# Performance work log

Measured on AMD Instinct MI355X. Metric: run time of the kernel, lower is better.

## Reference

```python
import jax, jax.numpy as jnp
import numpy as np

B = 4096
N_PATCH = 196  # 14x14 patches of a 28x28 image
THRESHOLD = 0.9
SECONDARY = 0.5
SECONDARY_WEIGHT = 0.5

_CNOT = jnp.array([[1, 0, 0, 0], [0, 1, 0, 0], [0, 0, 0, 1], [0, 0, 1, 0]], dtype=jnp.complex64)


def _ry(t):
    c, s = jnp.cos(t / 2), jnp.sin(t / 2)
    m = jnp.stack([jnp.stack([c, -s], -1), jnp.stack([s, c], -1)], -2)
    return m.astype(jnp.complex64)


def _rx(t):
    c, s = jnp.cos(t / 2), jnp.sin(t / 2)
    z = jnp.zeros_like(c)
    re = jnp.stack([jnp.stack([c, z], -1), jnp.stack([z, c], -1)], -2)
    im = jnp.stack([jnp.stack([z, -s], -1), jnp.stack([-s, z], -1)], -2)
    return (re + 1j * im).astype(jnp.complex64)


def _rz(t):
    em = jnp.exp(-0.5j * t.astype(jnp.complex64) if hasattr(t, 'astype') else -0.5j * t)
    ep = jnp.conj(em)
    z = jnp.zeros_like(em)
    m = jnp.stack([jnp.stack([em, z], -1), jnp.stack([z, ep], -1)], -2)
    return m.astype(jnp.complex64)


def _apply_1q(state, mat, wire):
    # state: (P, 2, 2, 2, 2); mat: (2,2) shared or (P,2,2) per-sample
    s = jnp.moveaxis(state, 1 + wire, -1)
    if mat.ndim == 2:
        s = jnp.einsum('pabcj,ij->pabci', s, mat)
    else:
        s = jnp.einsum('pabcj,pij->pabci', s, mat)
    return jnp.moveaxis(s, -1, 1 + wire)


def _apply_2q(state, mat4, w0, w1):
    s = jnp.moveaxis(state, (1 + w0, 1 + w1), (-2, -1))
    shp = s.shape
    s = s.reshape(shp[:-2] + (4,))
    s = jnp.einsum('...j,ij->...i', s, mat4)
    return jnp.moveaxis(s.reshape(shp), (-2, -1), (1 + w0, 1 + w1))


def _quantum_measure(angles, q_params):
    # angles: (P, 4) real -> Pauli-Z expectations (P, 4)
    P = angles.shape[0]
    state = jnp.zeros((P, 2, 2, 2, 2), jnp.complex64).at[:, 0, 0, 0, 0].set(1.0)
    # GeneralEncoder: RY(pixel) on each wire
    for w in range(4):
        state = _apply_1q(state, _ry(angles[:, w]), w)
    # fixed 'RandomLayer' (8 ops, deterministic gate sequence, trainable params)
    state = _apply_1q(state, _rx(q_params[0]), 0)
    state = _apply_1q(state, _ry(q_params[1]), 1)
    state = _apply_1q(state, _rz(q_params[2]), 2)
    state = _apply_2q(state, _CNOT, 0, 1)
    state = _apply_1q(state, _rx(q_params[3]), 3)
    state = _apply_2q(state, _CNOT, 2, 3)
    state = _apply_1q(state, _ry(q_params[4]), 0)
    state = _apply_1q(state, _rz(q_params[5]), 3)
    probs = state.real ** 2 + state.imag ** 2
    exps = []
    for w in range(4):
        p = jnp.moveaxis(probs, 1 + w, 1)
        exps.append((p[:, 0] - p[:, 1]).reshape(P, -1).sum(-1))
    return jnp.stack(exps, -1)


def setup_inputs() -> dict:
    key = jax.random.key(0)
    k1, k2, k3, k4 = jax.random.split(key, 4)
    x = jax.random.uniform(k1, (B, 1, 28, 28), dtype=jnp.float32)
    q_params = jax.random.uniform(k2, (6,), dtype=jnp.float32) * 2.0 * np.pi
    W = jax.random.normal(k3, (10, 4 * 14 * 14), dtype=jnp.float32) * 0.03
    b = jax.random.normal(k4, (10,), dtype=jnp.float32) * 0.01
    return {"x": x, "q_params": q_params, "W": W, "b": b}


def reference(x, q_params, W, b):
    Bsz = x.shape[0]
    # extract 2x2 patches in (tl, tr, bl, br) order -> (B*196, 4)
    p = x[:, 0].reshape(Bsz, 14, 2, 14, 2)
    p = jnp.transpose(p, (0, 1, 3, 2, 4)).reshape(Bsz * N_PATCH, 4)
    meas = _quantum_measure(p, q_params).reshape(Bsz, N_PATCH, 4)
    # adjacency from cosine similarity of first sample's patch vectors
    v = meas[0]
    nrm = jnp.linalg.norm(v, axis=-1, keepdims=True)
    sim = (v @ v.T) / (nrm * nrm.T + 1e-12)
    adj = jnp.where(sim >= THRESHOLD, 1.0,
                    jnp.where(sim >= SECONDARY, SECONDARY_WEIGHT, 0.0)).astype(meas.dtype)
    agg = jnp.einsum('nm,bmd->bnd', adj, meas)
    logits = agg.reshape(Bsz, -1) @ W.T + b
    return jax.nn.log_softmax(logits, axis=-1)
```

## Files before the change

### kernel.cpp

```cpp
#include <hip/hip_runtime.h>
#include <hip/hip_bf16.h>


#define NP 196

__device__ __forceinline__ float quad3(const float* H, const float* wa,
                                       const float* wb) {
  return wa[0] * (H[0] * wb[0] + H[1] * wb[1] + H[2] * wb[2]) +
         wa[1] * (H[3] * wb[0] + H[4] * wb[1] + H[5] * wb[2]) +
         wa[2] * (H[6] * wb[0] + H[7] * wb[1] + H[8] * wb[2]);
}

__device__ __forceinline__ void build_H_all(const float* __restrict__ qp,
                                            float* __restrict__ H) {
  float qc[6], qs[6];
#pragma unroll
  for (int i = 0; i < 6; ++i) __sincosf(0.5f * qp[i], &qs[i], &qc[i]);
#pragma unroll
  for (int sub = 0; sub < 2; ++sub) {
    float Mr[4][4] = {}, Mi[4][4] = {};
    if (sub == 0) {
      Mr[0][0] = Mr[1][1] = Mr[2][2] = Mr[3][3] = qc[0];
      Mi[0][2] = Mi[2][0] = Mi[1][3] = Mi[3][1] = -qs[0];
#pragma unroll
      for (int j = 0; j < 4; ++j) {
        float a, b;
        a = Mr[0][j]; b = Mr[1][j]; Mr[0][j] = qc[1]*a - qs[1]*b; Mr[1][j] = qs[1]*a + qc[1]*b;
        a = Mi[0][j]; b = Mi[1][j]; Mi[0][j] = qc[1]*a - qs[1]*b; Mi[1][j] = qs[1]*a + qc[1]*b;
        a = Mr[2][j]; b = Mr[3][j]; Mr[2][j] = qc[1]*a - qs[1]*b; Mr[3][j] = qs[1]*a + qc[1]*b;
        a = Mi[2][j]; b = Mi[3][j]; Mi[2][j] = qc[1]*a - qs[1]*b; Mi[3][j] = qs[1]*a + qc[1]*b;
      }
#pragma unroll
      for (int j = 0; j < 4; ++j) {
        float r = Mr[2][j]; Mr[2][j] = Mr[3][j]; Mr[3][j] = r;
        float q = Mi[2][j]; Mi[2][j] = Mi[3][j]; Mi[3][j] = q;
      }
#pragma unroll
      for (int j = 0; j < 4; ++j) {
        float a, b;
        a = Mr[0][j]; b = Mr[2][j]; Mr[0][j] = qc[4]*a - qs[4]*b; Mr[2][j] = qs[4]*a + qc[4]*b;
        a = Mi[0][j]; b = Mi[2][j]; Mi[0][j] = qc[4]*a - qs[4]*b; Mi[2][j] = qs[4]*a + qc[4]*b;
        a = Mr[1][j]; b = Mr[3][j]; Mr[1][j] = qc[4]*a - qs[4]*b; Mr[3][j] = qs[4]*a + qc[4]*b;
        a = Mi[1][j]; b = Mi[3][j]; Mi[1][j] = qc[4]*a - qs[4]*b; Mi[3][j] = qs[4]*a + qc[4]*b;
      }
    } else {
      Mr[0][0] = Mr[1][1] = Mr[2][2] = Mr[3][3] = qc[2];
      Mi[0][0] = Mi[1][1] = -qs[2]; Mi[2][2] = Mi[3][3] = qs[2];
#pragma unroll
      for (int j = 0; j < 4; ++j) {
        float ra, ia, rb, ib;
        ra = Mr[0][j]; ia = Mi[0][j]; rb = Mr[1][j]; ib = Mi[1][j];
        Mr[0][j] = qc[3]*ra + qs[3]*ib;  Mi[0][j] = qc[3]*ia - qs[3]*rb;
        Mr[1][j] = qc[3]*rb + qs[3]*ia;  Mi[1][j] = qc[3]*ib - qs[3]*ra;
        ra = Mr[2][j]; ia = Mi[2][j]; rb = Mr[3][j]; ib = Mi[3][j];
        Mr[2][j] = qc[3]*ra + qs[3]*ib;  Mi[2][j] = qc[3]*ia - qs[3]*rb;
        Mr[3][j] = qc[3]*rb + qs[3]*ia;  Mi[3][j] = qc[3]*ib - qs[3]*ra;
      }
#pragma unroll
      for (int j = 0; j < 4; ++j) {
        float r = Mr[2][j]; Mr[2][j] = Mr[3][j]; Mr[3][j] = r;
        float q = Mi[2][j]; Mi[2][j] = Mi[3][j]; Mi[3][j] = q;
      }
#pragma unroll
      for (int r = 0; r < 4; ++r) {
        float sg = (r & 1) ? 1.0f : -1.0f;
#pragma unroll
        for (int j = 0; j < 4; ++j) {
          float re = Mr[r][j], im = Mi[r][j];
          Mr[r][j] = qc[5] * re - sg * qs[5] * im;
          Mi[r][j] = qc[5] * im + sg * qs[5] * re;
        }
      }
    }
#pragma unroll
    for (int d = 0; d < 2; ++d) {
      float G[4][4];
#pragma unroll
      for (int j = 0; j < 4; ++j)
#pragma unroll
        for (int k = 0; k < 4; ++k) {
          float g = 0.0f;
#pragma unroll
          for (int i = 0; i < 4; ++i) {
            float sg = (d == 0) ? ((i < 2) ? 1.f : -1.f)
                                : (((i & 1) == 0) ? 1.f : -1.f);
            g += sg * (Mr[i][j] * Mr[i][k] + Mi[i][j] * Mi[i][k]);
          }
          G[j][k] = g;
        }
      float* Hd = H + sub * 18 + d * 9;
      Hd[0] = G[0][0];       Hd[1] = 2.f * G[0][1];               Hd[2] = G[1][1];
      Hd[3] = 2.f * G[0][2]; Hd[4] = 2.f * (G[0][3] + G[1][2]);   Hd[5] = 2.f * G[1][3];
      Hd[6] = G[2][2];       Hd[7] = 2.f * G[2][3];               Hd[8] = G[3][3];
    }
  }
}

__device__ __forceinline__ void meas_patch(const float* __restrict__ xb, int p,
                                           const float* __restrict__ H,
                                           float* e) {
  int i = p / 14, j = p - 14 * i;
  float2 top = *(const float2*)(xb + 56 * i + 2 * j);
  float2 bot = *(const float2*)(xb + 56 * i + 28 + 2 * j);
  float c0, s0, c1, s1, c2, s2, c3, s3;
  __sincosf(0.5f * top.x, &s0, &c0);
  __sincosf(0.5f * top.y, &s1, &c1);
  __sincosf(0.5f * bot.x, &s2, &c2);
  __sincosf(0.5f * bot.y, &s3, &c3);
  float wA0[3] = {c0 * c0, c0 * s0, s0 * s0};
  float wA1[3] = {c1 * c1, c1 * s1, s1 * s1};
  float wB0[3] = {c2 * c2, c2 * s2, s2 * s2};
  float wB1[3] = {c3 * c3, c3 * s3, s3 * s3};
  e[0] = quad3(H, wA0, wA1);
  e[1] = quad3(H + 9, wA0, wA1);
  e[2] = quad3(H + 18, wB0, wB1);
  e[3] = quad3(H + 27, wB0, wB1);
}

__global__ __launch_bounds__(64, 1) void k_w2(const float* __restrict__ x,
                                              const float* __restrict__ qp,
                                              const float* __restrict__ W,
                                              float* __restrict__ W2,
                                              float* __restrict__ HG) {
  __shared__ float vs[NP][4];
  __shared__ float ns[NP];
  __shared__ float wrow[NP];
  int m = blockIdx.x, lane = threadIdx.x;

  float H[36];
  build_H_all(qp, H);

  if (m == 0 && lane == 0) {
#pragma unroll
    for (int i = 0; i < 36; ++i) HG[i] = H[i];
  }

#pragma unroll
  for (int r = 0; r < 4; ++r) {
    int p = lane + 64 * r;
    if (p < NP) {
      float e[4];
      meas_patch(x, p, H, e);
      vs[p][0] = e[0]; vs[p][1] = e[1]; vs[p][2] = e[2]; vs[p][3] = e[3];
      ns[p] = sqrtf(e[0]*e[0] + e[1]*e[1] + e[2]*e[2] + e[3]*e[3]);
    }
  }
  __syncthreads();
  float v0 = vs[m][0], v1 = vs[m][1], v2 = vs[m][2], v3 = vs[m][3];
  float nm = ns[m];
  for (int c = lane; c < NP; c += 64) {
    float dot = v0 * vs[c][0] + v1 * vs[c][1] + v2 * vs[c][2] + v3 * vs[c][3];
    float sim = dot / (nm * ns[c] + 1e-12f);
    wrow[c] = (sim >= 0.9f) ? 1.0f : ((sim >= 0.5f) ? 0.5f : 0.0f);
  }
  __syncthreads();
  if (lane < 40) {
    int k = lane >> 2, d = lane & 3;
    const float* Wk = W + k * 784 + d;
    float acc = 0.0f;
#pragma unroll 8
    for (int n = 0; n < NP; ++n) acc += wrow[n] * Wk[4 * n];
    W2[k * 784 + 4 * m + d] = acc;
  }
}

__global__ __launch_bounds__(256, 2) void k_main(const float* __restrict__ x,
                                                 const float* __restrict__ HG,
                                                 const float* __restrict__ bias,
                                                 const float* __restrict__ W2,
                                                 float* __restrict__ out,
                                                 int Bsz) {
  int t = threadIdx.x, wv = t >> 6, lane = t & 63;
  int b = blockIdx.x * 4 + wv;
  if (b >= Bsz) return;

  float H[36];
#pragma unroll
  for (int i = 0; i < 36; ++i) H[i] = HG[i];
  float bv[10];
#pragma unroll
  for (int k = 0; k < 10; ++k) bv[k] = bias[k];

  const float* xb = x + (size_t)b * 784;
  float acc[10];
#pragma unroll
  for (int k = 0; k < 10; ++k) acc[k] = 0.0f;

#pragma unroll
  for (int r = 0; r < 4; ++r) {
    int p = lane + 64 * r;
    if (p < NP) {
      float e[4];
      meas_patch(xb, p, H, e);
#pragma unroll
      for (int k = 0; k < 10; ++k) {
        float4 w = *(const float4*)(W2 + k * 784 + 4 * p);
        acc[k] += e[0] * w.x + e[1] * w.y + e[2] * w.z + e[3] * w.w;
      }
    }
  }
#pragma unroll
  for (int k = 0; k < 10; ++k)
#pragma unroll
    for (int off = 32; off; off >>= 1) acc[k] += __shfl_xor(acc[k], off);

  float lg[10], m = -1e30f;
#pragma unroll
  for (int k = 0; k < 10; ++k) { lg[k] = acc[k] + bv[k]; m = fmaxf(m, lg[k]); }
  float s = 0.0f;
#pragma unroll
  for (int k = 0; k < 10; ++k) s += __expf(lg[k] - m);
  float lse = m + __logf(s);
  if (lane < 10) {
    float sel = lg[0];
#pragma unroll
    for (int k = 1; k < 10; ++k) sel = (lane == k) ? lg[k] : sel;
    out[(size_t)b * 10 + lane] = sel - lse;
  }
}

extern "C" void kernel_launch(void* const* d_in, const int* in_sizes, int n_in,
                              void* d_out, int out_size, void* d_ws, size_t ws_size,
                              hipStream_t stream) {
  const float* x  = (const float*)d_in[0];
  const float* qp = (const float*)d_in[1];
  const float* W  = (const float*)d_in[2];
  const float* bi = (const float*)d_in[3];
  float* out = (float*)d_out;

  int Bsz = in_sizes[0] / 784;

  float* W2 = (float*)d_ws;
  float* HG = W2 + 7840;

  k_w2<<<NP, 64, 0, stream>>>(x, qp, W, W2, HG);
  k_main<<<(Bsz + 3) / 4, 256, 0, stream>>>(x, HG, bi, W2, out, Bsz);
}
```

Before: 93.67 us.

## Process two samples per wave and widen the adjacency-weight kernel to 256 threads

The main kernel now has each wave handle two batch samples, so every W2 float4 load serves two accumulations instead of one. The cross-lane shuffle reduction stops at 8 lanes and finishes in shared memory with a parallel log-softmax over lanes. The W2 precompute kernel uses 256 threads, splitting each 196-term dot product into four chunks that are combined in shared memory. The aim is to cut W2 memory traffic and shuffle count, at the cost of more registers per thread and an extra block-level barrier.

```diff
diff --git a/kernel.cpp b/kernel.cpp
--- a/kernel.cpp
+++ b/kernel.cpp
@@ -117,50 +117,54 @@
   e[3] = quad3(H + 27, wB0, wB1);
 }
 
-__global__ __launch_bounds__(64, 1) void k_w2(const float* __restrict__ x,
-                                              const float* __restrict__ qp,
-                                              const float* __restrict__ W,
-                                              float* __restrict__ W2,
-                                              float* __restrict__ HG) {
+__global__ __launch_bounds__(256, 1) void k_w2(const float* __restrict__ x,
+                                               const float* __restrict__ qp,
+                                               const float* __restrict__ W,
+                                               float* __restrict__ W2,
+                                               float* __restrict__ HG) {
   __shared__ float vs[NP][4];
   __shared__ float ns[NP];
   __shared__ float wrow[NP];
-  int m = blockIdx.x, lane = threadIdx.x;
+  __shared__ float red[160];
+  int m = blockIdx.x, t = threadIdx.x;
 
   float H[36];
   build_H_all(qp, H);
 
-  if (m == 0 && lane == 0) {
+  if (m == 0 && t == 0) {
 #pragma unroll
     for (int i = 0; i < 36; ++i) HG[i] = H[i];
   }
 
-#pragma unroll
-  for (int r = 0; r < 4; ++r) {
-    int p = lane + 64 * r;
-    if (p < NP) {
-      float e[4];
-      meas_patch(x, p, H, e);
-      vs[p][0] = e[0]; vs[p][1] = e[1]; vs[p][2] = e[2]; vs[p][3] = e[3];
-      ns[p] = sqrtf(e[0]*e[0] + e[1]*e[1] + e[2]*e[2] + e[3]*e[3]);
-    }
+  if (t < NP) {
+    float e[4];
+    meas_patch(x, t, H, e);
+    vs[t][0] = e[0]; vs[t][1] = e[1]; vs[t][2] = e[2]; vs[t][3] = e[3];
+    ns[t] = sqrtf(e[0]*e[0] + e[1]*e[1] + e[2]*e[2] + e[3]*e[3]);
   }
   __syncthreads();
   float v0 = vs[m][0], v1 = vs[m][1], v2 = vs[m][2], v3 = vs[m][3];
   float nm = ns[m];
-  for (int c = lane; c < NP; c += 64) {
-    float dot = v0 * vs[c][0] + v1 * vs[c][1] + v2 * vs[c][2] + v3 * vs[c][3];
-    float sim = dot / (nm * ns[c] + 1e-12f);
-    wrow[c] = (sim >= 0.9f) ? 1.0f : ((sim >= 0.5f) ? 0.5f : 0.0f);
-  }
-  __syncthreads();
-  if (lane < 40) {
-    int k = lane >> 2, d = lane & 3;
+  if (t < NP) {
+    float dot = v0 * vs[t][0] + v1 * vs[t][1] + v2 * vs[t][2] + v3 * vs[t][3];
+    float sim = dot / (nm * ns[t] + 1e-12f);
+    wrow[t] = (sim >= 0.9f) ? 1.0f : ((sim >= 0.5f) ? 0.5f : 0.0f);
+  }
+  __syncthreads();
+  if (t < 160) {
+    int pair = t >> 2, chunk = t & 3;
+    int k = pair >> 2, d = pair & 3;
     const float* Wk = W + k * 784 + d;
     float acc = 0.0f;
-#pragma unroll 8
-    for (int n = 0; n < NP; ++n) acc += wrow[n] * Wk[4 * n];
-    W2[k * 784 + 4 * m + d] = acc;
+    int n0 = chunk * 49;
+#pragma unroll 7
+    for (int n = n0; n < n0 + 49; ++n) acc += wrow[n] * Wk[4 * n];
+    red[t] = acc;
+  }
+  __syncthreads();
+  if (t < 40) {
+    int k = t >> 2, d = t & 3;
+    W2[k * 784 + 4 * m + d] = red[4*t] + red[4*t+1] + red[4*t+2] + red[4*t+3];
   }
 }
 
@@ -170,53 +174,74 @@
                                                  const float* __restrict__ W2,
                                                  float* __restrict__ out,
                                                  int Bsz) {
+  __shared__ float red[4][160];
   int t = threadIdx.x, wv = t >> 6, lane = t & 63;
-  int b = blockIdx.x * 4 + wv;
-  if (b >= Bsz) return;
+  int b0 = blockIdx.x * 8 + wv * 2;
+  bool vA = b0 < Bsz, vB = (b0 + 1) < Bsz;
 
   float H[36];
 #pragma unroll
   for (int i = 0; i < 36; ++i) H[i] = HG[i];
-  float bv[10];
-#pragma unroll
-  for (int k = 0; k < 10; ++k) bv[k] = bias[k];
-
-  const float* xb = x + (size_t)b * 784;
-  float acc[10];
-#pragma unroll
-  for (int k = 0; k < 10; ++k) acc[k] = 0.0f;
+
+  const float* xa = x + (size_t)b0 * 784;
+  const float* xb = xa + 784;
+  float accA[10], accB[10];
+#pragma unroll
+  for (int k = 0; k < 10; ++k) { accA[k] = 0.0f; accB[k] = 0.0f; }
 
 #pragma unroll
   for (int r = 0; r < 4; ++r) {
     int p = lane + 64 * r;
     if (p < NP) {
-      float e[4];
-      meas_patch(xb, p, H, e);
+      float eA[4] = {0.f, 0.f, 0.f, 0.f};
+      float eB[4] = {0.f, 0.f, 0.f, 0.f};
+      if (vA) meas_patch(xa, p, H, eA);
+      if (vB) meas_patch(xb, p, H, eB);
 #pragma unroll
       for (int k = 0; k < 10; ++k) {
         float4 w = *(const float4*)(W2 + k * 784 + 4 * p);
-        acc[k] += e[0] * w.x + e[1] * w.y + e[2] * w.z + e[3] * w.w;
-      }
-    }
-  }
-#pragma unroll
-  for (int k = 0; k < 10; ++k)
-#pragma unroll
-    for (int off = 32; off; off >>= 1) acc[k] += __shfl_xor(acc[k], off);
-
-  float lg[10], m = -1e30f;
-#pragma unroll
-  for (int k = 0; k < 10; ++k) { lg[k] = acc[k] + bv[k]; m = fmaxf(m, lg[k]); }
-  float s = 0.0f;
-#pragma unroll
-  for (int k = 0; k < 10; ++k) s += __expf(lg[k] - m);
-  float lse = m + __logf(s);
-  if (lane < 10) {
-    float sel = lg[0];
-#pragma unroll
-    for (int k = 1; k < 10; ++k) sel = (lane == k) ? lg[k] : sel;
-    out[(size_t)b * 10 + lane] = sel - lse;
-  }
+        accA[k] += eA[0] * w.x + eA[1] * w.y + eA[2] * w.z + eA[3] * w.w;
+        accB[k] += eB[0] * w.x + eB[1] * w.y + eB[2] * w.z + eB[3] * w.w;
+      }
+    }
+  }
+
+#pragma unroll
+  for (int k = 0; k < 10; ++k) {
+#pragma unroll
+    for (int off = 32; off >= 8; off >>= 1) {
+      accA[k] += __shfl_xor(accA[k], off);
+      accB[k] += __shfl_xor(accB[k], off);
+    }
+  }
+  if (lane < 8) {
+#pragma unroll
+    for (int k = 0; k < 10; ++k) {
+      red[wv][k * 8 + lane]      = accA[k];
+      red[wv][80 + k * 8 + lane] = accB[k];
+    }
+  }
+  __syncthreads();
+
+  int s = lane >> 5;
+  int k10 = lane & 31;
+  float lg = -1e30f;
+  if (k10 < 10) {
+    const float4* q = (const float4*)&red[wv][s * 80 + k10 * 8];
+    float4 a = q[0], b4 = q[1];
+    lg = ((a.x + a.y) + (a.z + a.w)) + ((b4.x + b4.y) + (b4.z + b4.w)) +
+         bias[k10];
+  }
+  float mx = lg;
+#pragma unroll
+  for (int off = 8; off; off >>= 1) mx = fmaxf(mx, __shfl_xor(mx, off));
+  float ex = (k10 < 10) ? __expf(lg - mx) : 0.0f;
+  float sm = ex;
+#pragma unroll
+  for (int off = 8; off; off >>= 1) sm += __shfl_xor(sm, off);
+  float lse = mx + __logf(sm);
+  bool vs_ = s ? vB : vA;
+  if (k10 < 10 && vs_) out[(size_t)(b0 + s) * 10 + k10] = lg - lse;
 }
 
 extern "C" void kernel_launch(void* const* d_in, const int* in_sizes, int n_in,
@@ -233,6 +258,6 @@
   float* W2 = (float*)d_ws;
   float* HG = W2 + 7840;
 
-  k_w2<<<NP, 64, 0, stream>>>(x, qp, W, W2, HG);
-  k_main<<<(Bsz + 3) / 4, 256, 0, stream>>>(x, HG, bi, W2, out, Bsz);
-}
+  k_w2<<<NP, 256, 0, stream>>>(x, qp, W, W2, HG);
+  k_main<<<(Bsz + 7) / 8, 256, 0, stream>>>(x, HG, bi, W2, out, Bsz);
+}
```

Result: faster. 77.17 us (-17.6%).
